# Kernel optimization log

Measured on AMD Instinct MI355X. Metric: run time of the kernel, lower is better.

The kernel has to match this reference:

```python
import jax, jax.numpy as jnp
import numpy as np

N_MOL, E_MOL = 50000, 200000
N_PRO, E_PRO = 100000, 800000


def segment_softmax(e, seg, n):
    # e: [E, H] logits, softmax over edges grouped by target node `seg`
    m = jax.ops.segment_max(e, seg, num_segments=n)
    m = jnp.where(jnp.isfinite(m), m, jnp.zeros_like(m))
    ex = jnp.exp(e - m[seg])
    s = jax.ops.segment_sum(ex, seg, num_segments=n)
    return ex / (s[seg] + 1e-16)


def gat_conv(x, edge_index, W, a_src, a_dst, b, heads, out_ch):
    # torch_geometric GATConv (concat=True, add_self_loops=True, neg slope 0.2, eval mode)
    n = x.shape[0]
    loop = jnp.arange(n, dtype=edge_index.dtype)
    src = jnp.concatenate([edge_index[0], loop])
    dst = jnp.concatenate([edge_index[1], loop])
    h = (x @ W).reshape(n, heads, out_ch)            # [N,H,C]
    alpha_s = jnp.sum(h * a_src, axis=-1)            # [N,H]
    alpha_d = jnp.sum(h * a_dst, axis=-1)            # [N,H]
    e = jax.nn.leaky_relu(alpha_s[src] + alpha_d[dst], 0.2)  # [E,H]
    alpha = segment_softmax(e, dst, n)               # [E,H]
    out = jax.ops.segment_sum(alpha[:, :, None] * h[src], dst, num_segments=n)  # [N,H,C]
    return out.reshape(n, heads * out_ch) + b


def gcn_conv(x, edge_index, edge_weight, W, b):
    # torch_geometric GCNConv with edge_weight (add_self_loops=True, sym norm)
    n = x.shape[0]
    loop = jnp.arange(n, dtype=edge_index.dtype)
    src = jnp.concatenate([edge_index[0], loop])
    dst = jnp.concatenate([edge_index[1], loop])
    w = jnp.concatenate([edge_weight, jnp.ones((n,), x.dtype)])
    deg = jax.ops.segment_sum(w, dst, num_segments=n)
    dinv = jnp.where(deg > 0, deg ** -0.5, jnp.zeros_like(deg))
    norm = dinv[src] * w * dinv[dst]                 # [E]
    h = x @ W                                        # [N,C]
    return jax.ops.segment_sum(norm[:, None] * h[src], dst, num_segments=n) + b


def setup_inputs() -> dict:
    key = jax.random.key(0)
    ks = iter(jax.random.split(key, 32))
    rn = lambda shape, s=0.1: jax.random.normal(next(ks), shape, dtype=jnp.float32) * s
    inp = {
        "mol_x": rn((N_MOL, 78), 1.0),
        "mol_edge_index": jax.random.randint(next(ks), (2, E_MOL), 0, N_MOL, dtype=jnp.int32),
        "pro_x": rn((N_PRO, 33), 1.0),
        "pro_edge_index": jax.random.randint(next(ks), (2, E_PRO), 0, N_PRO, dtype=jnp.int32),
        "pro_edge_weight": jax.random.uniform(next(ks), (E_PRO,), dtype=jnp.float32),
        # mol_conv1: GAT 78->78, heads=2
        "W1": rn((78, 156)), "a_src1": rn((2, 78)), "a_dst1": rn((2, 78)), "b1": jnp.zeros((156,), jnp.float32),
        # mol_conv2: GAT 156->156, heads=2
        "W2": rn((156, 312)), "a_src2": rn((2, 156)), "a_dst2": rn((2, 156)), "b2": jnp.zeros((312,), jnp.float32),
        # mol_conv3: GAT 312->312, heads=1
        "W3": rn((312, 312)), "a_src3": rn((1, 312)), "a_dst3": rn((1, 312)), "b3": jnp.zeros((312,), jnp.float32),
        # pro_conv1: GCN 33->33
        "Wp1": rn((33, 33)), "bp1": jnp.zeros((33,), jnp.float32),
        # pro_conv2: GAT 33->66, heads=2
        "Wp2": rn((33, 132)), "ap_src2": rn((2, 66)), "ap_dst2": rn((2, 66)), "bp2": jnp.zeros((132,), jnp.float32),
        # pro_conv3: GAT 132->132, heads=1
        "Wp3": rn((132, 132)), "ap_src3": rn((1, 132)), "ap_dst3": rn((1, 132)), "bp3": jnp.zeros((132,), jnp.float32),
    }
    return inp


def reference(mol_x, mol_edge_index, pro_x, pro_edge_index, pro_edge_weight,
              W1, a_src1, a_dst1, b1, W2, a_src2, a_dst2, b2, W3, a_src3, a_dst3, b3,
              Wp1, bp1, Wp2, ap_src2, ap_dst2, bp2, Wp3, ap_src3, ap_dst3, bp3):
    # mol branch (per CPI_GAT.forward): conv1 -> relu -> conv2 -> relu -> conv3
    x = jax.nn.relu(gat_conv(mol_x, mol_edge_index, W1, a_src1, a_dst1, b1, 2, 78))
    x = jax.nn.relu(gat_conv(x, mol_edge_index, W2, a_src2, a_dst2, b2, 2, 156))
    x = gat_conv(x, mol_edge_index, W3, a_src3, a_dst3, b3, 1, 312)
    # pro branch: gcn -> relu -> gat -> relu -> gat -> relu
    xt = jax.nn.relu(gcn_conv(pro_x, pro_edge_index, pro_edge_weight, Wp1, bp1))
    xt = jax.nn.relu(gat_conv(xt, pro_edge_index, Wp2, ap_src2, ap_dst2, bp2, 2, 66))
    xt = jax.nn.relu(gat_conv(xt, pro_edge_index, Wp3, ap_src3, ap_dst3, bp3, 1, 132))
    return (x, xt)
```

## Files before the change

kernel.cpp:

```cpp
#include <hip/hip_runtime.h>
#include <cstdint>
#include <cstddef>

#define WAVE 64
#define NPB 4

#define TBM 128
#define TBN 128
#define TBK 32
#define LDK 40

typedef short s16x8 __attribute__((ext_vector_type(8)));
typedef float f32x4 __attribute__((ext_vector_type(4)));

__device__ __forceinline__ unsigned short f2bf(float f) {
    unsigned int u = __float_as_uint(f);
    unsigned int r = (u + 0x7fffu + ((u >> 16) & 1u)) >> 16;
    return (unsigned short)r;
}
__device__ __forceinline__ float bf2f_lo(unsigned int v) { return __uint_as_float(v << 16); }
__device__ __forceinline__ float bf2f_hi(unsigned int v) { return __uint_as_float(v & 0xffff0000u); }
__device__ __forceinline__ float lrelu02(float e) { return (e > 0.f) ? e : 0.2f * e; }


__device__ __forceinline__ void gemm_body(const unsigned short* __restrict__ A,
                                          const unsigned short* __restrict__ BT,
                                          unsigned short* __restrict__ Cbf,
                                          float* __restrict__ asb, float* __restrict__ adb,
                                          const float* __restrict__ bias, int relu, int zpadTo,
                                          int N, int Kp, int M, int Mext, int Mp, int H,
                                          int bx, int by) {
    __shared__ __align__(16) unsigned short As[TBM * LDK];
    __shared__ __align__(16) unsigned short Bs[TBN * LDK];
    int tid = threadIdx.x;
    int wave = tid >> 6;
    int lane = tid & 63;
    int rowBase = by * TBM;
    int colBase = bx * TBN;
    int wm = (wave & 1) * 64;
    int wn = (wave >> 1) * 64;
    int l15 = lane & 15;
    int quad = lane >> 4;

    f32x4 acc[4][4];
    f32x4 z4 = {0.f, 0.f, 0.f, 0.f};
#pragma unroll
    for (int i = 0; i < 4; i++)
#pragma unroll
        for (int j = 0; j < 4; j++) acc[i][j] = z4;

    int srow = tid >> 2;
    int skg = tid & 3;
    const uint4 zero16 = {0u, 0u, 0u, 0u};

    for (int k0 = 0; k0 < Kp; k0 += TBK) {
#pragma unroll
        for (int half = 0; half < 2; half++) {
            int row = srow + half * 64;
            int gk = k0 + skg * 8;
            bool kok = (gk < Kp);
            {
                int gr = rowBase + row;
                uint4 v = zero16;
                if (kok && gr < N) v = *(const uint4*)(A + (size_t)gr * Kp + gk);
                *(uint4*)(As + row * LDK + skg * 8) = v;
            }
            {
                int gc = colBase + row;
                uint4 v = zero16;
                if (kok && gc < Mext) v = *(const uint4*)(BT + (size_t)gc * Kp + gk);
                *(uint4*)(Bs + row * LDK + skg * 8) = v;
            }
        }
        __syncthreads();

        s16x8 af[4], bfr[4];
#pragma unroll
        for (int mt = 0; mt < 4; mt++)
            af[mt] = *(const s16x8*)(As + (wm + mt * 16 + l15) * LDK + quad * 8);
#pragma unroll
        for (int nt = 0; nt < 4; nt++)
            bfr[nt] = *(const s16x8*)(Bs + (wn + nt * 16 + l15) * LDK + quad * 8);
#pragma unroll
        for (int mt = 0; mt < 4; mt++)
#pragma unroll
            for (int nt = 0; nt < 4; nt++)
                acc[mt][nt] = __builtin_amdgcn_mfma_f32_16x16x32_bf16(af[mt], bfr[nt], acc[mt][nt], 0, 0, 0);
        __syncthreads();
    }

#pragma unroll
    for (int mt = 0; mt < 4; mt++) {
#pragma unroll
        for (int r = 0; r < 4; r++) {
            int row = rowBase + wm + mt * 16 + quad * 4 + r;
            if (row < N) {
#pragma unroll
                for (int nt = 0; nt < 4; nt++) {
                    int col = colBase + wn + nt * 16 + l15;
                    float v = acc[mt][nt][r];
                    if (col < M) {
                        float v2 = v;
                        if (bias != nullptr) {
                            v2 += bias[col];
                            if (relu) v2 = fmaxf(v2, 0.f);
                        }
                        Cbf[(size_t)row * Mp + col] = f2bf(v2);
                    } else if (col < zpadTo) {
                        Cbf[(size_t)row * Mp + col] = 0;
                    } else if (asb != nullptr && col < M + 2 * H) {
                        int t = col - M;
                        if (t < H) asb[(size_t)row * H + t] = v;
                        else adb[(size_t)row * H + (t - H)] = v;
                    }
                }
            }
        }
    }
}


template <int SLOTS, int NG, int H, bool SM, int SWEEPS, bool GCN, bool NEXTA>
__device__ __forceinline__ void agg_gp(const unsigned short* __restrict__ hfeat,
                                       const float* __restrict__ as_, const float* __restrict__ ad_,
                                       const float* __restrict__ dinv,
                                       const int* __restrict__ rowp, const int2* __restrict__ cpack,
                                       const float* __restrict__ bias,
                                       float* __restrict__ out_f, unsigned short* __restrict__ out_bf,
                                       const float* __restrict__ vanf, int vald,
                                       float* __restrict__ asn, float* __restrict__ adn_o,
                                       int HC, int ldo, int relu, int nbase, int lane, int N) {
    constexpr int ROWB = SWEEPS * SLOTS * 16;
    int g = lane / SLOTS;
    int slot = lane - g * SLOTS;
    int n = nbase + g;
    if (g >= NG || n >= N) return;
    int C = HC / H;
    int beg = rowp[n], end = rowp[n + 1];

    float adn[H], msub[H];
    float di = 0.f, sfw;
    if (GCN) {
        di = dinv[n];
        sfw = di * di;
    } else {
#pragma unroll
        for (int h = 0; h < H; h++) {
            adn[h] = ad_[(size_t)n * H + h];
            msub[h] = lrelu02(as_[(size_t)n * H + h] + adn[h]);
        }
        sfw = 1.f;
    }

    int ch0[SWEEPS];
    bool h1q[SWEEPS][4];
#pragma unroll
    for (int sw = 0; sw < SWEEPS; sw++) {
        ch0[sw] = (sw * SLOTS + slot) * 8;
#pragma unroll
        for (int q = 0; q < 4; q++) h1q[sw][q] = (H == 2) && ((ch0[sw] + 2 * q) >= C);
    }

    float accx[SWEEPS][4], accy[SWEEPS][4];
#pragma unroll
    for (int sw = 0; sw < SWEEPS; sw++) {
        uint4 v = *(const uint4*)((const char*)hfeat + (size_t)n * ROWB + (sw * SLOTS + slot) * 16);
        unsigned int vv[4] = {v.x, v.y, v.z, v.w};
#pragma unroll
        for (int q = 0; q < 4; q++) { accx[sw][q] = sfw * bf2f_lo(vv[q]); accy[sw][q] = sfw * bf2f_hi(vv[q]); }
    }

    float wsum[H];
#pragma unroll
    for (int h = 0; h < H; h++) wsum[h] = 0.f;

    int p = beg;
    for (; p + 1 < end; p += 2) {
        int2 pk0 = cpack[p];
        int2 pk1 = cpack[p + 1];
        int s0 = pk0.x, s1 = pk1.x;
        float w0[H], w1[H];
        if (GCN) {
            w0[0] = dinv[s0] * __int_as_float(pk0.y) * di;
            w1[0] = dinv[s1] * __int_as_float(pk1.y) * di;
        } else {
#pragma unroll
            for (int h = 0; h < H; h++) {
                w0[h] = __expf(lrelu02(as_[(size_t)s0 * H + h] + adn[h]) - msub[h]);
                w1[h] = __expf(lrelu02(as_[(size_t)s1 * H + h] + adn[h]) - msub[h]);
            }
        }
        if (SM) {
#pragma unroll
            for (int h = 0; h < H; h++) wsum[h] += w0[h] + w1[h];
        }
        uint4 v0[SWEEPS], v1[SWEEPS];
#pragma unroll
        for (int sw = 0; sw < SWEEPS; sw++)
            v0[sw] = *(const uint4*)((const char*)hfeat + (size_t)s0 * ROWB + (sw * SLOTS + slot) * 16);
#pragma unroll
        for (int sw = 0; sw < SWEEPS; sw++)
            v1[sw] = *(const uint4*)((const char*)hfeat + (size_t)s1 * ROWB + (sw * SLOTS + slot) * 16);
#pragma unroll
        for (int sw = 0; sw < SWEEPS; sw++) {
            unsigned int a0[4] = {v0[sw].x, v0[sw].y, v0[sw].z, v0[sw].w};
            unsigned int a1[4] = {v1[sw].x, v1[sw].y, v1[sw].z, v1[sw].w};
#pragma unroll
            for (int q = 0; q < 4; q++) {
                float wq0 = (H == 2) ? (h1q[sw][q] ? w0[1] : w0[0]) : w0[0];
                float wq1 = (H == 2) ? (h1q[sw][q] ? w1[1] : w1[0]) : w1[0];
                accx[sw][q] += wq0 * bf2f_lo(a0[q]) + wq1 * bf2f_lo(a1[q]);
                accy[sw][q] += wq0 * bf2f_hi(a0[q]) + wq1 * bf2f_hi(a1[q]);
            }
        }
    }
    if (p < end) {
        int2 pk0 = cpack[p];
        int s0 = pk0.x;
        float w0[H];
        if (GCN) {
            w0[0] = dinv[s0] * __int_as_float(pk0.y) * di;
        } else {
#pragma unroll
            for (int h = 0; h < H; h++)
                w0[h] = __expf(lrelu02(as_[(size_t)s0 * H + h] + adn[h]) - msub[h]);
        }
        if (SM) {
#pragma unroll
            for (int h = 0; h < H; h++) wsum[h] += w0[h];
        }
        uint4 v0[SWEEPS];
#pragma unroll
        for (int sw = 0; sw < SWEEPS; sw++)
            v0[sw] = *(const uint4*)((const char*)hfeat + (size_t)s0 * ROWB + (sw * SLOTS + slot) * 16);
#pragma unroll
        for (int sw = 0; sw < SWEEPS; sw++) {
            unsigned int a0[4] = {v0[sw].x, v0[sw].y, v0[sw].z, v0[sw].w};
#pragma unroll
            for (int q = 0; q < 4; q++) {
                float wq0 = (H == 2) ? (h1q[sw][q] ? w0[1] : w0[0]) : w0[0];
                accx[sw][q] += wq0 * bf2f_lo(a0[q]);
                accy[sw][q] += wq0 * bf2f_hi(a0[q]);
            }
        }
    }

    float rs[H];
    if (SM) {
#pragma unroll
        for (int h = 0; h < H; h++) rs[h] = 1.f / (1.f + wsum[h] + 1e-16f);
    } else {
#pragma unroll
        for (int h = 0; h < H; h++) rs[h] = 1.f;
    }

    float ps[4] = {0.f, 0.f, 0.f, 0.f};
#pragma unroll
    for (int sw = 0; sw < SWEEPS; sw++) {
        float o[8];
#pragma unroll
        for (int q = 0; q < 4; q++) {
            float r = (H == 2) ? (h1q[sw][q] ? rs[1] : rs[0]) : rs[0];
            int c0 = ch0[sw] + 2 * q;
            float b0 = (c0 < HC) ? bias[c0] : 0.f;
            float b1v = (c0 + 1 < HC) ? bias[c0 + 1] : 0.f;
            float o0 = accx[sw][q] * r + b0;
            float o1 = accy[sw][q] * r + b1v;
            if (relu) { o0 = fmaxf(o0, 0.f); o1 = fmaxf(o1, 0.f); }
            if (c0 >= HC) o0 = 0.f;
            if (c0 + 1 >= HC) o1 = 0.f;
            o[2 * q] = o0;
            o[2 * q + 1] = o1;
        }
        if (NEXTA) {
#pragma unroll
            for (int j = 0; j < 8; j++) {
                int c = ch0[sw] + j;
#pragma unroll
                for (int th = 0; th < 4; th++) ps[th] += o[j] * vanf[th * vald + c];
            }
        }
        if (out_bf) {
            uint4 pk;
            unsigned* pp = (unsigned*)&pk;
#pragma unroll
            for (int q = 0; q < 4; q++)
                pp[q] = (unsigned)f2bf(o[2 * q]) | ((unsigned)f2bf(o[2 * q + 1]) << 16);
            *(uint4*)((char*)out_bf + (size_t)n * ((size_t)ldo * 2) + (sw * SLOTS + slot) * 16) = pk;
        } else {
#pragma unroll
            for (int half = 0; half < 2; half++) {
                int c0 = ch0[sw] + half * 4;
                if (c0 < HC) {
                    float4 f4 = make_float4(o[half * 4], o[half * 4 + 1], o[half * 4 + 2], o[half * 4 + 3]);
                    *(float4*)(out_f + (size_t)n * HC + c0) = f4;
                }
            }
        }
    }
    if (NEXTA) {
        constexpr int P = SLOTS >= 32 ? 32 : SLOTS >= 16 ? 16 : SLOTS >= 8 ? 8 : SLOTS >= 4 ? 4 : SLOTS >= 2 ? 2 : 1;
        if (P < SLOTS) {
#pragma unroll
            for (int th = 0; th < 4; th++) {
                float t = __shfl_down(ps[th], P);
                if (slot + P < SLOTS) ps[th] += t;
            }
        }
#pragma unroll
        for (int off = P >> 1; off > 0; off >>= 1) {
#pragma unroll
            for (int th = 0; th < 4; th++) {
                float t = __shfl_down(ps[th], off);
                if (slot + off < P) ps[th] += t;
            }
        }
        if (slot == 0) {
            asn[(size_t)n * 2 + 0] = ps[0];
            asn[(size_t)n * 2 + 1] = ps[1];
            adn_o[(size_t)n * 2 + 0] = ps[2];
            adn_o[(size_t)n * 2 + 1] = ps[3];
        }
    }
}


template <int SLOTS, int NG>
__device__ __forceinline__ void aggN_gp(const unsigned short* __restrict__ x,
                                        const float* __restrict__ as_, const float* __restrict__ ad_,
                                        const int* __restrict__ rowp, const int2* __restrict__ cpack,
                                        unsigned short* __restrict__ A2, int nbase, int lane, int N) {
    constexpr int ROWB = SLOTS * 16;
    int g = lane / SLOTS;
    int slot = lane - g * SLOTS;
    int n = nbase + g;
    if (g >= NG || n >= N) return;
    int beg = rowp[n], end = rowp[n + 1];

    float adn[2], msub[2];
#pragma unroll
    for (int h = 0; h < 2; h++) {
        adn[h] = ad_[(size_t)n * 2 + h];
        msub[h] = lrelu02(as_[(size_t)n * 2 + h] + adn[h]);
    }

    float ax[2][4], ay[2][4];
    {
        uint4 v = *(const uint4*)((const char*)x + (size_t)n * ROWB + slot * 16);
        unsigned int vv[4] = {v.x, v.y, v.z, v.w};
#pragma unroll
        for (int q = 0; q < 4; q++) {
            float lo = bf2f_lo(vv[q]), hi = bf2f_hi(vv[q]);
            ax[0][q] = lo; ax[1][q] = lo;
            ay[0][q] = hi; ay[1][q] = hi;
        }
    }
    float wsum[2] = {0.f, 0.f};

    int p = beg;
    for (; p + 1 < end; p += 2) {
        int s0 = cpack[p].x;
        int s1 = cpack[p + 1].x;
        float w0[2], w1[2];
#pragma unroll
        for (int h = 0; h < 2; h++) {
            w0[h] = __expf(lrelu02(as_[(size_t)s0 * 2 + h] + adn[h]) - msub[h]);
            w1[h] = __expf(lrelu02(as_[(size_t)s1 * 2 + h] + adn[h]) - msub[h]);
        }
        wsum[0] += w0[0] + w1[0];
        wsum[1] += w0[1] + w1[1];
        uint4 v0 = *(const uint4*)((const char*)x + (size_t)s0 * ROWB + slot * 16);
        uint4 v1 = *(const uint4*)((const char*)x + (size_t)s1 * ROWB + slot * 16);
        unsigned int a0[4] = {v0.x, v0.y, v0.z, v0.w};
        unsigned int a1[4] = {v1.x, v1.y, v1.z, v1.w};
#pragma unroll
        for (int q = 0; q < 4; q++) {
            float lo0 = bf2f_lo(a0[q]), hi0 = bf2f_hi(a0[q]);
            float lo1 = bf2f_lo(a1[q]), hi1 = bf2f_hi(a1[q]);
            ax[0][q] += w0[0] * lo0 + w1[0] * lo1;
            ax[1][q] += w0[1] * lo0 + w1[1] * lo1;
            ay[0][q] += w0[0] * hi0 + w1[0] * hi1;
            ay[1][q] += w0[1] * hi0 + w1[1] * hi1;
        }
    }
    if (p < end) {
        int s0 = cpack[p].x;
        float w0[2];
#pragma unroll
        for (int h = 0; h < 2; h++)
            w0[h] = __expf(lrelu02(as_[(size_t)s0 * 2 + h] + adn[h]) - msub[h]);
        wsum[0] += w0[0];
        wsum[1] += w0[1];
        uint4 v0 = *(const uint4*)((const char*)x + (size_t)s0 * ROWB + slot * 16);
        unsigned int a0[4] = {v0.x, v0.y, v0.z, v0.w};
#pragma unroll
        for (int q = 0; q < 4; q++) {
            float lo0 = bf2f_lo(a0[q]), hi0 = bf2f_hi(a0[q]);
            ax[0][q] += w0[0] * lo0;
            ax[1][q] += w0[1] * lo0;
            ay[0][q] += w0[0] * hi0;
            ay[1][q] += w0[1] * hi0;
        }
    }

    float rs[2];
#pragma unroll
    for (int h = 0; h < 2; h++) rs[h] = 1.f / (1.f + wsum[h] + 1e-16f);

#pragma unroll
    for (int h = 0; h < 2; h++) {
        uint4 pk;
        unsigned* pp = (unsigned*)&pk;
#pragma unroll
        for (int q = 0; q < 4; q++) {
            float o0 = ax[h][q] * rs[h];
            float o1 = ay[h][q] * rs[h];
            pp[q] = (unsigned)f2bf(o0) | ((unsigned)f2bf(o1) << 16);
        }
        *(uint4*)((char*)A2 + (size_t)n * (2 * ROWB) + h * ROWB + slot * 16) = pk;
    }
}


__device__ __forceinline__ void cvtw1(const float* __restrict__ W, unsigned short* __restrict__ WT,
                                      int K, int M, int Kp, int i) {
    int m = i / Kp;
    int k = i - m * Kp;
    WT[i] = (k < K) ? f2bf(W[(long long)k * M + m]) : (unsigned short)0;
}

__device__ __forceinline__ void cvtw_bd(const float* __restrict__ W, unsigned short* __restrict__ WT,
                                        int K, int M, int C, int Kp, int Kph, int i) {
    int m = i / Kp;
    int k = i - m * Kp;
    unsigned short v = 0;
    if (m < M) {
        int hm = m / C;
        int kk = k - hm * Kph;
        if (kk >= 0 && kk < K) v = f2bf(W[(long long)kk * M + m]);
    }
    WT[i] = v;
}

__device__ __forceinline__ void prep1(const float* __restrict__ W, const float* __restrict__ a_src,
                                      const float* __restrict__ a_dst, unsigned short* __restrict__ WT,
                                      int K, int M, int C, int Kp, int H, int b, int lane) {
    int k = b % Kp;
    int th = b / Kp;
    int t = th / H;
    int h = th - t * H;
    size_t orow = (size_t)(M + t * H + h) * Kp;
    if (k >= K) {
        if (lane == 0) WT[orow + k] = 0;
        return;
    }
    const float* a = t ? a_dst : a_src;
    int hoff = h * C;
    const float* wrow = W + (size_t)k * M + hoff;
    float acc = 0.f;
    for (int c = lane; c < C; c += 64) acc += wrow[c] * a[hoff + c];
    for (int off = 32; off > 0; off >>= 1) acc += __shfl_down(acc, off);
    if (lane == 0) WT[orow + k] = f2bf(acc);
}

__device__ __forceinline__ void prep1f(const float* __restrict__ W, const float* __restrict__ a_src,
                                       const float* __restrict__ a_dst, float* __restrict__ fout,
                                       int K, int M, int C, int Kp, int H, int b, int lane) {
    int k = b % Kp;
    int th = b / Kp;
    int t = th / H;
    int h = th - t * H;
    if (k >= K) {
        if (lane == 0) fout[(size_t)th * Kp + k] = 0.f;
        return;
    }
    const float* a = t ? a_dst : a_src;
    int hoff = h * C;
    const float* wrow = W + (size_t)k * M + hoff;
    float acc = 0.f;
    for (int c = lane; c < C; c += 64) acc += wrow[c] * a[hoff + c];
    for (int off = 32; off > 0; off >>= 1) acc += __shfl_down(acc, off);
    if (lane == 0) fout[(size_t)th * Kp + k] = acc;
}


__global__ __launch_bounds__(256) void k_A(
    const int* __restrict__ mol_dst, const int* __restrict__ pro_dst, int* __restrict__ cnt,
    int N_MOL, int E_MOL, int ET, int nb1,
    const float* __restrict__ W1, const float* __restrict__ W2, const float* __restrict__ W3,
    const float* __restrict__ Wp1, const float* __restrict__ Wp2, const float* __restrict__ Wp3,
    unsigned short* __restrict__ wt1, unsigned short* __restrict__ wt2bd, unsigned short* __restrict__ wt3,
    unsigned short* __restrict__ wtp1, unsigned short* __restrict__ wtp2bd, unsigned short* __restrict__ wtp3,
    const float* __restrict__ as1, const float* __restrict__ ad1,
    const float* __restrict__ as2, const float* __restrict__ ad2,
    const float* __restrict__ as3, const float* __restrict__ ad3,
    const float* __restrict__ aps2, const float* __restrict__ apd2,
    const float* __restrict__ aps3, const float* __restrict__ apd3,
    float* __restrict__ va2f, float* __restrict__ vap2f,
    const float* __restrict__ mol_x, unsigned short* __restrict__ xb,
    const float* __restrict__ pro_x, unsigned short* __restrict__ xpp,
    long long totM, long long totP) {
    const int nb2 = 957;
    const int nb3 = 508;
    int b = blockIdx.x;
    int tid = threadIdx.x;
    if (b < nb1) {
        int i0 = b * 1024 + tid;
#pragma unroll
        for (int k = 0; k < 4; k++) {
            int e = i0 + k * 256;
            if (e < ET) {
                int d = (e < E_MOL) ? mol_dst[e] : (N_MOL + pro_dst[e - E_MOL]);
                atomicAdd(&cnt[d], 1);
            }
        }
    } else if (b < nb1 + nb2) {
        int idx = (b - nb1) * 256 + tid;
        if (idx < 12480)        cvtw1(W1, wt1, 78, 156, 80, idx);
        else if (idx < 114880)  cvtw_bd(W2, wt2bd, 156, 312, 156, 320, 160, idx - 12480);
        else if (idx < 214720)  cvtw1(W3, wt3, 312, 312, 320, idx - 114880);
        else if (idx < 216040)  cvtw1(Wp1, wtp1, 33, 33, 40, idx - 214720);
        else if (idx < 226920)  cvtw_bd(Wp2, wtp2bd, 33, 132, 66, 80, 40, idx - 216040);
        else if (idx < 244872)  cvtw1(Wp3, wtp3, 132, 132, 136, idx - 226920);
    } else if (b < nb1 + nb2 + nb3) {
        int unit = (b - nb1 - nb2) * 4 + (tid >> 6);
        int lane = tid & 63;
        if (unit < 320)        prep1(W1, as1, ad1, wt1, 78, 156, 78, 80, 2, unit, lane);
        else if (unit < 960)   prep1f(W2, as2, ad2, va2f, 156, 312, 156, 160, 2, unit - 320, lane);
        else if (unit < 1600)  prep1(W3, as3, ad3, wt3, 312, 312, 312, 320, 1, unit - 960, lane);
        else if (unit < 1760)  prep1f(Wp2, aps2, apd2, vap2f, 33, 132, 66, 40, 2, unit - 1600, lane);
        else if (unit < 2032)  prep1(Wp3, aps3, apd3, wtp3, 132, 132, 132, 136, 1, unit - 1760, lane);
    } else {
        long long i0 = (long long)(b - nb1 - nb2 - nb3) * 1024 + tid;
#pragma unroll
        for (int k = 0; k < 4; k++) {
            long long idx = i0 + k * 256;
            if (idx < totM) {
                int n = (int)(idx / 80);
                int kk = (int)(idx - (long long)n * 80);
                xb[idx] = (kk < 78) ? f2bf(mol_x[(long long)n * 78 + kk]) : (unsigned short)0;
            } else if (idx < totM + totP) {
                long long i2 = idx - totM;
                int n = (int)(i2 / 40);
                int kk = (int)(i2 - (long long)n * 40);
                xpp[i2] = (kk < 33) ? f2bf(pro_x[(long long)n * 33 + kk]) : (unsigned short)0;
            }
        }
    }
}


__global__ __launch_bounds__(256) void k_scan1(const int* __restrict__ cnt, int* __restrict__ incl,
                                               int* __restrict__ bsums, int n) {
    __shared__ int sm[256];
    int i = blockIdx.x * 256 + threadIdx.x;
    int v = (i < n) ? cnt[i] : 0;
    sm[threadIdx.x] = v;
    __syncthreads();
    for (int off = 1; off < 256; off <<= 1) {
        int t = (threadIdx.x >= off) ? sm[threadIdx.x - off] : 0;
        __syncthreads();
        sm[threadIdx.x] += t;
        __syncthreads();
    }
    if (i < n) incl[i] = sm[threadIdx.x];
    if (threadIdx.x == 255) bsums[blockIdx.x] = sm[255];
}

__global__ __launch_bounds__(1024) void k_scan2(int* __restrict__ bsums, int nb) {
    __shared__ int sm[1024];
    int v = (threadIdx.x < nb) ? bsums[threadIdx.x] : 0;
    sm[threadIdx.x] = v;
    __syncthreads();
    for (int off = 1; off < 1024; off <<= 1) {
        int t = (threadIdx.x >= off) ? sm[threadIdx.x - off] : 0;
        __syncthreads();
        sm[threadIdx.x] += t;
        __syncthreads();
    }
    if (threadIdx.x < nb) bsums[threadIdx.x] = sm[threadIdx.x] - v;
}

__global__ __launch_bounds__(256) void k_scan3_all(const int* __restrict__ incl, const int* __restrict__ cnt,
                                                   const int* __restrict__ boff,
                                                   int* __restrict__ mol_rowp, int* __restrict__ pro_rowp,
                                                   int* __restrict__ cur,
                                                   int N_MOL, int N_PRO, int E_MOL, int E_PRO) {
    int i = blockIdx.x * 256 + threadIdx.x;
    int NT = N_MOL + N_PRO;
    if (i < NT) {
        int ex = incl[i] - cnt[i] + boff[blockIdx.x];
        cur[i] = ex;
        if (i < N_MOL) mol_rowp[i] = ex;
        else pro_rowp[i - N_MOL] = ex - E_MOL;
    }
    if (i == 0) {
        mol_rowp[N_MOL] = E_MOL;
        pro_rowp[N_PRO] = E_PRO;
    }
}


__global__ __launch_bounds__(256) void k_B(
    const int* __restrict__ msrc, const int* __restrict__ mdst,
    const int* __restrict__ psrc, const int* __restrict__ pdst,
    const float* __restrict__ pw, int* __restrict__ cur, int2* __restrict__ cpack,
    int N_MOL, int E_MOL, int ET, int nbs,
    const unsigned short* __restrict__ A1, const unsigned short* __restrict__ B1,
    unsigned short* __restrict__ C1, float* __restrict__ as1o, float* __restrict__ ad1o,
    const float* __restrict__ bias1, int relu1, int zpad1,
    int N1, int Kp1, int M1, int Mext1, int Mp1, int H1, int g1x, int nb1,
    const unsigned short* __restrict__ A2, const unsigned short* __restrict__ B2,
    unsigned short* __restrict__ C2, float* __restrict__ as2o, float* __restrict__ ad2o,
    const float* __restrict__ bias2, int relu2, int zpad2,
    int N2, int Kp2, int M2, int Mext2, int Mp2, int H2, int g2x) {
    int b = blockIdx.x;
    if (b < nbs) {
        int e = b * 256 + threadIdx.x;
        if (e < ET) {
            int s, d;
            int wbits = 0;
            if (e >= E_MOL) {
                int ep = e - E_MOL;
                s = psrc[ep];
                d = N_MOL + pdst[ep];
                wbits = __float_as_int(pw[ep]);
            } else {
                s = msrc[e];
                d = mdst[e];
            }
            int pos = atomicAdd(&cur[d], 1);
            int2 pk;
            pk.x = s;
            pk.y = wbits;
            cpack[pos] = pk;
        }
    } else if (b < nbs + nb1) {
        int bb = b - nbs;
        gemm_body(A1, B1, C1, as1o, ad1o, bias1, relu1, zpad1, N1, Kp1, M1, Mext1, Mp1, H1, bb % g1x, bb / g1x);
    } else {
        int bb = b - nbs - nb1;
        gemm_body(A2, B2, C2, as2o, ad2o, bias2, relu2, zpad2, N2, Kp2, M2, Mext2, Mp2, H2, bb % g2x, bb / g2x);
    }
}


__global__ __launch_bounds__(256) void k_deg(const int* __restrict__ rowp, const int2* __restrict__ cpack,
                                             float* __restrict__ dinv, int N) {
    int n = blockIdx.x * 256 + threadIdx.x;
    if (n < N) {
        int b = rowp[n], e = rowp[n + 1];
        float s = 0.f;
        for (int p = b; p < e; p++) s += __int_as_float(cpack[p].y);
        dinv[n] = rsqrtf(s + 1.0f);
    }
}


__global__ __launch_bounds__(NPB * 64) void k_fuse1(
    const unsigned short* __restrict__ hb, const float* __restrict__ asm_, const float* __restrict__ adm_,
    const int* __restrict__ mrowp, const int2* __restrict__ mcp, const float* __restrict__ b1,
    unsigned short* __restrict__ x2m, const float* __restrict__ va2f,
    float* __restrict__ asm2, float* __restrict__ adm2, int Nm,
    const unsigned short* __restrict__ hbp, const float* __restrict__ dinv,
    const int* __restrict__ prowp, const int2* __restrict__ pcp, const float* __restrict__ bp1,
    unsigned short* __restrict__ x2p, const float* __restrict__ vap2f,
    float* __restrict__ asp2, float* __restrict__ adp2, int Np, int nb1) {
    int wave = threadIdx.x >> 6, lane = threadIdx.x & 63;
    int b = blockIdx.x;
    if (b < nb1) {
        int nbase = (b * NPB + wave) * 3;
        agg_gp<20, 3, 2, true, 1, false, true>(hb, asm_, adm_, nullptr, mrowp, mcp, b1,
                                               nullptr, x2m, va2f, 160, asm2, adm2,
                                               156, 160, 1, nbase, lane, Nm);
    } else {
        int nbase = ((b - nb1) * NPB + wave) * 12;
        agg_gp<5, 12, 1, false, 1, true, true>(hbp, nullptr, nullptr, dinv, prowp, pcp, bp1,
                                               nullptr, x2p, vap2f, 40, asp2, adp2,
                                               33, 40, 1, nbase, lane, Np);
    }
}

__global__ __launch_bounds__(NPB * 64) void k_fuseN(
    const unsigned short* __restrict__ x2m, const float* __restrict__ asm2, const float* __restrict__ adm2,
    const int* __restrict__ mrowp, const int2* __restrict__ mcp, unsigned short* __restrict__ xa2m, int Nm,
    const unsigned short* __restrict__ x2p, const float* __restrict__ asp2, const float* __restrict__ adp2,
    const int* __restrict__ prowp, const int2* __restrict__ pcp, unsigned short* __restrict__ xa2p, int Np,
    int nb1) {
    int wave = threadIdx.x >> 6, lane = threadIdx.x & 63;
    int b = blockIdx.x;
    if (b < nb1) {
        int nbase = (b * NPB + wave) * 3;
        aggN_gp<20, 3>(x2m, asm2, adm2, mrowp, mcp, xa2m, nbase, lane, Nm);
    } else {
        int nbase = ((b - nb1) * NPB + wave) * 12;
        aggN_gp<5, 12>(x2p, asp2, adp2, prowp, pcp, xa2p, nbase, lane, Np);
    }
}

__global__ __launch_bounds__(NPB * 64) void k_fuse5(
    const unsigned short* __restrict__ hb, const float* __restrict__ asm_, const float* __restrict__ adm_,
    const int* __restrict__ mrowp, const int2* __restrict__ mcp, const float* __restrict__ b3,
    float* __restrict__ out_mol, int Nm,
    const unsigned short* __restrict__ hbp, const float* __restrict__ asp_, const float* __restrict__ adp_,
    const int* __restrict__ prowp, const int2* __restrict__ pcp, const float* __restrict__ bp3,
    float* __restrict__ out_pro, int Np, int nb1) {
    int wave = threadIdx.x >> 6, lane = threadIdx.x & 63;
    int b = blockIdx.x;
    if (b < nb1) {
        int nbase = (b * NPB + wave) * 3;
        agg_gp<20, 3, 1, true, 2, false, false>(hb, asm_, adm_, nullptr, mrowp, mcp, b3,
                                                out_mol, nullptr, nullptr, 0, nullptr, nullptr,
                                                312, 320, 0, nbase, lane, Nm);
    } else {
        int nbase = ((b - nb1) * NPB + wave) * 3;
        agg_gp<17, 3, 1, true, 1, false, false>(hbp, asp_, adp_, nullptr, prowp, pcp, bp3,
                                                out_pro, nullptr, nullptr, 0, nullptr, nullptr,
                                                132, 136, 1, nbase, lane, Np);
    }
}


extern "C" void kernel_launch(void* const* d_in, const int* in_sizes, int n_in,
                              void* d_out, int out_size, void* d_ws, size_t ws_size,
                              hipStream_t stream) {
    const int N_MOL = in_sizes[0] / 78;
    const int E_MOL = in_sizes[1] / 2;
    const int N_PRO = in_sizes[2] / 33;
    const int E_PRO = in_sizes[3] / 2;
    const int NT = N_MOL + N_PRO;
    const int ET = E_MOL + E_PRO;

    const float* mol_x = (const float*)d_in[0];
    const int* mol_ei = (const int*)d_in[1];
    const float* pro_x = (const float*)d_in[2];
    const int* pro_ei = (const int*)d_in[3];
    const float* pro_ew = (const float*)d_in[4];
    const float *W1 = (const float*)d_in[5], *as1 = (const float*)d_in[6], *ad1 = (const float*)d_in[7],
                *b1 = (const float*)d_in[8];
    const float *W2 = (const float*)d_in[9], *as2 = (const float*)d_in[10], *ad2 = (const float*)d_in[11],
                *b2 = (const float*)d_in[12];
    const float *W3 = (const float*)d_in[13], *as3 = (const float*)d_in[14], *ad3 = (const float*)d_in[15],
                *b3 = (const float*)d_in[16];
    const float *Wp1 = (const float*)d_in[17], *bp1 = (const float*)d_in[18];
    const float *Wp2 = (const float*)d_in[19], *aps2 = (const float*)d_in[20], *apd2 = (const float*)d_in[21],
                *bp2 = (const float*)d_in[22];
    const float *Wp3 = (const float*)d_in[23], *aps3 = (const float*)d_in[24], *apd3 = (const float*)d_in[25],
                *bp3 = (const float*)d_in[26];

    float* out_mol = (float*)d_out;
    float* out_pro = (float*)d_out + (size_t)N_MOL * 312;

    char* ob = (char*)d_out;
    size_t o_xa2m = 0;
    size_t o_xa2p = o_xa2m + (size_t)N_MOL * 320 * 2;
    size_t o_xb0  = o_xa2p + (size_t)N_PRO * 80 * 2;
    size_t o_xp0  = o_xb0 + (size_t)N_MOL * 80 * 2;
    size_t o_xpp  = o_xp0 + (size_t)N_PRO * 40 * 2;
    unsigned short* xa2m = (unsigned short*)(ob + o_xa2m);
    unsigned short* xa2p = (unsigned short*)(ob + o_xa2p);
    unsigned short* xb0  = (unsigned short*)(ob + o_xb0);
    unsigned short* xp0  = (unsigned short*)(ob + o_xp0);
    unsigned short* xpp  = (unsigned short*)(ob + o_xpp);

    char* p = (char*)d_ws;
    auto alloc = [&](size_t bytes) -> void* {
        void* r = (void*)p;
        p += (bytes + 255) & ~(size_t)255;
        return r;
    };
    int* cnt_all  = (int*)alloc((size_t)NT * 4);
    int* incl     = (int*)alloc((size_t)NT * 4);
    int* cur_all  = (int*)alloc((size_t)NT * 4);
    int* bsums    = (int*)alloc(1024 * 4);
    int* mol_rowp = (int*)alloc((size_t)(N_MOL + 1) * 4);
    int* pro_rowp = (int*)alloc((size_t)(N_PRO + 1) * 4);
    int2* cpack   = (int2*)alloc((size_t)ET * 8);
    float* dinv   = (float*)alloc((size_t)N_PRO * 4);
    float* asb_m  = (float*)alloc((size_t)N_MOL * 2 * 4);
    float* adb_m  = (float*)alloc((size_t)N_MOL * 2 * 4);
    float* asb_m2 = (float*)alloc((size_t)N_MOL * 2 * 4);
    float* adb_m2 = (float*)alloc((size_t)N_MOL * 2 * 4);
    float* asb_p  = (float*)alloc((size_t)N_PRO * 2 * 4);
    float* adb_p  = (float*)alloc((size_t)N_PRO * 2 * 4);
    float* asb_p2 = (float*)alloc((size_t)N_PRO * 2 * 4);
    float* adb_p2 = (float*)alloc((size_t)N_PRO * 2 * 4);
    float* va2f   = (float*)alloc((size_t)4 * 160 * 4);
    float* vap2f  = (float*)alloc((size_t)4 * 40 * 4);
    unsigned short* bufA = (unsigned short*)alloc((size_t)N_MOL * 320 * 2);
    unsigned short* bufB = (unsigned short*)alloc((size_t)N_MOL * 320 * 2);
    unsigned short* bufC = (unsigned short*)alloc((size_t)N_PRO * 136 * 2);
    unsigned short* wt1    = (unsigned short*)alloc((size_t)160 * 80 * 2);
    unsigned short* wt2bd  = (unsigned short*)alloc((size_t)320 * 320 * 2);
    unsigned short* wt3    = (unsigned short*)alloc((size_t)320 * 320 * 2);
    unsigned short* wtp1   = (unsigned short*)alloc((size_t)40 * 40 * 2);
    unsigned short* wtp2bd = (unsigned short*)alloc((size_t)136 * 80 * 2);
    unsigned short* wtp3   = (unsigned short*)alloc((size_t)136 * 136 * 2);
    (void)ws_size;

    unsigned short* hb1  = bufA;
    unsigned short* x3m  = bufA;
    unsigned short* x2m  = bufB;
    unsigned short* x2p  = bufB + (size_t)N_MOL * 160;
    unsigned short* hb3  = bufB;
    unsigned short* hbp1 = bufC;
    unsigned short* hbp3 = bufC;

    int2* mol_cp = cpack;
    int2* pro_cp = cpack + E_MOL;

    const int* mol_src = mol_ei;
    const int* mol_dst = mol_ei + E_MOL;
    const int* pro_src = pro_ei;
    const int* pro_dst = pro_ei + E_PRO;

    const long long totM = (long long)N_MOL * 80;
    const long long totP = (long long)N_PRO * 40;

    hipMemsetAsync(cnt_all, 0, (size_t)NT * 4, stream);
    int nbCnt = (ET + 1023) / 1024;
    int nbCvx = (int)((totM + totP + 1023) / 1024);
    int gridA = nbCnt + 957 + 508 + nbCvx;
    k_A<<<gridA, 256, 0, stream>>>(mol_dst, pro_dst, cnt_all, N_MOL, E_MOL, ET, nbCnt,
                                   W1, W2, W3, Wp1, Wp2, Wp3, wt1, wt2bd, wt3, wtp1, wtp2bd, wtp3,
                                   as1, ad1, as2, ad2, as3, ad3, aps2, apd2, aps3, apd3,
                                   va2f, vap2f, mol_x, xb0, pro_x, xp0, totM, totP);

    int nbT = (NT + 255) / 256;
    k_scan1<<<nbT, 256, 0, stream>>>(cnt_all, incl, bsums, NT);
    k_scan2<<<1, 1024, 0, stream>>>(bsums, nbT);
    k_scan3_all<<<nbT, 256, 0, stream>>>(incl, cnt_all, bsums, mol_rowp, pro_rowp, cur_all,
                                         N_MOL, N_PRO, E_MOL, E_PRO);

    int gyM = (N_MOL + TBM - 1) / TBM;
    int gyP = (N_PRO + TBM - 1) / TBM;

    {
        int nbs = (ET + 255) / 256;
        int g1x = 2;
        int nb1 = g1x * gyM;
        int g2x = 1;
        k_B<<<nbs + nb1 + g2x * gyP, 256, 0, stream>>>(
            mol_src, mol_dst, pro_src, pro_dst, pro_ew, cur_all, cpack, N_MOL, E_MOL, ET, nbs,
            xb0, wt1, hb1, asb_m, adb_m, nullptr, 0, 0, N_MOL, 80, 156, 160, 160, 2, g1x, nb1,
            xp0, wtp1, hbp1, nullptr, nullptr, nullptr, 0, 0, N_PRO, 40, 33, 33, 40, 0, g2x);
    }

    k_deg<<<(N_PRO + 255) / 256, 256, 0, stream>>>(pro_rowp, pro_cp, dinv, N_PRO);

    {
        int nb1 = (N_MOL + NPB * 3 - 1) / (NPB * 3);
        int nb2 = (N_PRO + NPB * 12 - 1) / (NPB * 12);
        k_fuse1<<<nb1 + nb2, NPB * 64, 0, stream>>>(hb1, asb_m, adb_m, mol_rowp, mol_cp, b1,
                                                    x2m, va2f, asb_m2, adb_m2, N_MOL,
                                                    hbp1, dinv, pro_rowp, pro_cp, bp1,
                                                    x2p, vap2f, asb_p2, adb_p2, N_PRO, nb1);
    }

    {
        int nb1 = (N_MOL + NPB * 3 - 1) / (NPB * 3);
        int nb2 = (N_PRO + NPB * 12 - 1) / (NPB * 12);
        k_fuseN<<<nb1 + nb2, NPB * 64, 0, stream>>>(x2m, asb_m2, adb_m2, mol_rowp, mol_cp, xa2m, N_MOL,
                                                    x2p, asb_p2, adb_p2, pro_rowp, pro_cp, xa2p, N_PRO, nb1);
    }

    {
        int g1x = 3;
        int nb1 = g1x * gyM;
        int g2x = 2;
        k_B<<<nb1 + g2x * gyP, 256, 0, stream>>>(
            nullptr, nullptr, nullptr, nullptr, nullptr, nullptr, nullptr, N_MOL, E_MOL, ET, 0,
            xa2m, wt2bd, x3m, nullptr, nullptr, b2, 1, 320, N_MOL, 320, 312, 320, 320, 0, g1x, nb1,
            xa2p, wtp2bd, xpp, nullptr, nullptr, bp2, 1, 136, N_PRO, 80, 132, 136, 136, 0, g2x);
    }

    {
        int g1x = 3;
        int nb1 = g1x * gyM;
        int g2x = 2;
        k_B<<<nb1 + g2x * gyP, 256, 0, stream>>>(
            nullptr, nullptr, nullptr, nullptr, nullptr, nullptr, nullptr, N_MOL, E_MOL, ET, 0,
            x3m, wt3, hb3, asb_m, adb_m, nullptr, 0, 0, N_MOL, 320, 312, 314, 320, 1, g1x, nb1,
            xpp, wtp3, hbp3, asb_p, adb_p, nullptr, 0, 0, N_PRO, 136, 132, 134, 136, 1, g2x);
    }

    {
        int nb1 = (N_MOL + NPB * 3 - 1) / (NPB * 3);
        int nb2 = (N_PRO + NPB * 3 - 1) / (NPB * 3);
        k_fuse5<<<nb1 + nb2, NPB * 64, 0, stream>>>(hb3, asb_m, adb_m, mol_rowp, mol_cp, b3, out_mol, N_MOL,
                                                    hbp3, asb_p, adb_p, pro_rowp, pro_cp, bp3, out_pro, N_PRO, nb1);
    }
}
```

Before: 707.1 us.

## Replace direct CSR edge scatter with two-pass bucketed scatter

After: 694.9 us, median of 2. Within noise of the previous version (-1.7%).

```diff
diff --git a/kernel.cpp b/kernel.cpp
--- a/kernel.cpp
+++ b/kernel.cpp
@@ -487,6 +487,7 @@
 __global__ __launch_bounds__(256) void k_A(
     const int* __restrict__ mol_dst, const int* __restrict__ pro_dst, int* __restrict__ cnt,
     int N_MOL, int E_MOL, int ET, int nb1,
+    int* __restrict__ hist, int NBLK, int NBUK, int SH, int ROUNDS,
     const float* __restrict__ W1, const float* __restrict__ W2, const float* __restrict__ W3,
     const float* __restrict__ Wp1, const float* __restrict__ Wp2, const float* __restrict__ Wp3,
     unsigned short* __restrict__ wt1, unsigned short* __restrict__ wt2bd, unsigned short* __restrict__ wt3,
@@ -504,6 +505,7 @@
     const int nb3 = 508;
     int b = blockIdx.x;
     int tid = threadIdx.x;
+    __shared__ int lhist[256];
     if (b < nb1) {
         int i0 = b * 1024 + tid;
 #pragma unroll
@@ -514,16 +516,30 @@
                 atomicAdd(&cnt[d], 1);
             }
         }
-    } else if (b < nb1 + nb2) {
-        int idx = (b - nb1) * 256 + tid;
+    } else if (b < nb1 + NBLK) {
+        int eb = b - nb1;
+        lhist[tid] = 0;
+        __syncthreads();
+        int base = eb * (ROUNDS * 256);
+        for (int r = 0; r < ROUNDS; r++) {
+            int e = base + r * 256 + tid;
+            if (e < ET) {
+                int d = (e < E_MOL) ? mol_dst[e] : (N_MOL + pro_dst[e - E_MOL]);
+                atomicAdd(&lhist[d >> SH], 1);
+            }
+        }
+        __syncthreads();
+        if (tid < NBUK) hist[tid * NBLK + eb] = lhist[tid];
+    } else if (b < nb1 + NBLK + nb2) {
+        int idx = (b - nb1 - NBLK) * 256 + tid;
         if (idx < 12480)        cvtw1(W1, wt1, 78, 156, 80, idx);
         else if (idx < 114880)  cvtw_bd(W2, wt2bd, 156, 312, 156, 320, 160, idx - 12480);
         else if (idx < 214720)  cvtw1(W3, wt3, 312, 312, 320, idx - 114880);
         else if (idx < 216040)  cvtw1(Wp1, wtp1, 33, 33, 40, idx - 214720);
         else if (idx < 226920)  cvtw_bd(Wp2, wtp2bd, 33, 132, 66, 80, 40, idx - 216040);
         else if (idx < 244872)  cvtw1(Wp3, wtp3, 132, 132, 136, idx - 226920);
-    } else if (b < nb1 + nb2 + nb3) {
-        int unit = (b - nb1 - nb2) * 4 + (tid >> 6);
+    } else if (b < nb1 + NBLK + nb2 + nb3) {
+        int unit = (b - nb1 - NBLK - nb2) * 4 + (tid >> 6);
         int lane = tid & 63;
         if (unit < 320)        prep1(W1, as1, ad1, wt1, 78, 156, 78, 80, 2, unit, lane);
         else if (unit < 960)   prep1f(W2, as2, ad2, va2f, 156, 312, 156, 160, 2, unit - 320, lane);
@@ -531,7 +547,7 @@
         else if (unit < 1760)  prep1f(Wp2, aps2, apd2, vap2f, 33, 132, 66, 40, 2, unit - 1600, lane);
         else if (unit < 2032)  prep1(Wp3, aps3, apd3, wtp3, 132, 132, 132, 136, 1, unit - 1760, lane);
     } else {
-        long long i0 = (long long)(b - nb1 - nb2 - nb3) * 1024 + tid;
+        long long i0 = (long long)(b - nb1 - NBLK - nb2 - nb3) * 1024 + tid;
 #pragma unroll
         for (int k = 0; k < 4; k++) {
             long long idx = i0 + k * 256;
@@ -601,11 +617,31 @@
 }
 
 
+__global__ __launch_bounds__(256) void k_histscan(int* __restrict__ hist, const int* __restrict__ cur,
+                                                  int NBLK, int SH, int NT, int ET) {
+    __shared__ int sm[256];
+    int b = blockIdx.x;
+    int t = threadIdx.x;
+    int v = (t < NBLK) ? hist[b * NBLK + t] : 0;
+    sm[t] = v;
+    __syncthreads();
+    for (int off = 1; off < 256; off <<= 1) {
+        int x = (t >= off) ? sm[t - off] : 0;
+        __syncthreads();
+        sm[t] += x;
+        __syncthreads();
+    }
+    int node = b << SH;
+    int base = (node < NT) ? cur[node] : ET;
+    if (t < NBLK) hist[b * NBLK + t] = base + sm[t] - v;
+}
+
+
 __global__ __launch_bounds__(256) void k_B(
     const int* __restrict__ msrc, const int* __restrict__ mdst,
     const int* __restrict__ psrc, const int* __restrict__ pdst,
-    const float* __restrict__ pw, int* __restrict__ cur, int2* __restrict__ cpack,
-    int N_MOL, int E_MOL, int ET, int nbs,
+    const float* __restrict__ pw, const int* __restrict__ blockstart, int2* __restrict__ ebkt,
+    int N_MOL, int E_MOL, int ET, int nbs, int NBLK, int NBUK, int SH, int ROUNDS,
     const unsigned short* __restrict__ A1, const unsigned short* __restrict__ B1,
     unsigned short* __restrict__ C1, float* __restrict__ as1o, float* __restrict__ ad1o,
     const float* __restrict__ bias1, int relu1, int zpad1,
@@ -616,24 +652,33 @@
     int N2, int Kp2, int M2, int Mext2, int Mp2, int H2, int g2x) {
     int b = blockIdx.x;
     if (b < nbs) {
-        int e = b * 256 + threadIdx.x;
-        if (e < ET) {
-            int s, d;
-            int wbits = 0;
-            if (e >= E_MOL) {
-                int ep = e - E_MOL;
-                s = psrc[ep];
-                d = N_MOL + pdst[ep];
-                wbits = __float_as_int(pw[ep]);
-            } else {
-                s = msrc[e];
-                d = mdst[e];
-            }
-            int pos = atomicAdd(&cur[d], 1);
-            int2 pk;
-            pk.x = s;
-            pk.y = wbits;
-            cpack[pos] = pk;
+        __shared__ int lofs[256];
+        int eb = b;
+        int tid = threadIdx.x;
+        if (tid < NBUK) lofs[tid] = blockstart[tid * NBLK + eb];
+        __syncthreads();
+        int base = eb * (ROUNDS * 256);
+        for (int r = 0; r < ROUNDS; r++) {
+            int e = base + r * 256 + tid;
+            if (e < ET) {
+                int s, d;
+                int wbits = 0;
+                if (e >= E_MOL) {
+                    int ep = e - E_MOL;
+                    s = psrc[ep];
+                    d = N_MOL + pdst[ep];
+                    wbits = __float_as_int(pw[ep]);
+                } else {
+                    s = msrc[e];
+                    d = mdst[e];
+                }
+                int bk = d >> SH;
+                int pos = atomicAdd(&lofs[bk], 1);
+                int2 pk;
+                pk.x = s | ((d - (bk << SH)) << 18);
+                pk.y = wbits;
+                ebkt[pos] = pk;
+            }
         }
     } else if (b < nbs + nb1) {
         int bb = b - nbs;
@@ -641,6 +686,26 @@
     } else {
         int bb = b - nbs - nb1;
         gemm_body(A2, B2, C2, as2o, ad2o, bias2, relu2, zpad2, N2, Kp2, M2, Mext2, Mp2, H2, bb % g2x, bb / g2x);
+    }
+}
+
+
+__global__ __launch_bounds__(256) void k_pass2(const int2* __restrict__ ebkt, const int* __restrict__ blockstart,
+                                               int* __restrict__ cur, int2* __restrict__ cpack,
+                                               int NBUK, int NBLK, int SH, int ET) {
+    int b = blockIdx.x >> 3;
+    int s = blockIdx.x & 7;
+    int start = blockstart[b * NBLK];
+    int end = (b + 1 < NBUK) ? blockstart[(b + 1) * NBLK] : ET;
+    for (int i = start + s * 256 + threadIdx.x; i < end; i += 8 * 256) {
+        int2 pk = ebkt[i];
+        int src = pk.x & 0x3FFFF;
+        int d = (b << SH) | ((unsigned)pk.x >> 18);
+        int pos = atomicAdd(&cur[d], 1);
+        int2 o;
+        o.x = src;
+        o.y = pk.y;
+        cpack[pos] = o;
     }
 }
 
@@ -751,6 +816,14 @@
     float* out_mol = (float*)d_out;
     float* out_pro = (float*)d_out + (size_t)N_MOL * 312;
 
+    int SH = 10;
+    while (((NT + (1 << SH) - 1) >> SH) > 256) SH++;
+    const int NBUK = (NT + (1 << SH) - 1) >> SH;
+    int ROUNDS = (ET + 65535) / 65536;
+    if (ROUNDS < 16) ROUNDS = 16;
+    const int EB = ROUNDS * 256;
+    const int NBLK = (ET + EB - 1) / EB;
+
     char* ob = (char*)d_out;
     size_t o_xa2m = 0;
     size_t o_xa2p = o_xa2m + (size_t)N_MOL * 320 * 2;
@@ -776,6 +849,8 @@
     int* mol_rowp = (int*)alloc((size_t)(N_MOL + 1) * 4);
     int* pro_rowp = (int*)alloc((size_t)(N_PRO + 1) * 4);
     int2* cpack   = (int2*)alloc((size_t)ET * 8);
+    int2* ebkt    = (int2*)alloc((size_t)ET * 8);
+    int* hist     = (int*)alloc((size_t)256 * 256 * 4);
     float* dinv   = (float*)alloc((size_t)N_PRO * 4);
     float* asb_m  = (float*)alloc((size_t)N_MOL * 2 * 4);
     float* adb_m  = (float*)alloc((size_t)N_MOL * 2 * 4);
@@ -820,8 +895,9 @@
     hipMemsetAsync(cnt_all, 0, (size_t)NT * 4, stream);
     int nbCnt = (ET + 1023) / 1024;
     int nbCvx = (int)((totM + totP + 1023) / 1024);
-    int gridA = nbCnt + 957 + 508 + nbCvx;
+    int gridA = nbCnt + NBLK + 957 + 508 + nbCvx;
     k_A<<<gridA, 256, 0, stream>>>(mol_dst, pro_dst, cnt_all, N_MOL, E_MOL, ET, nbCnt,
+                                   hist, NBLK, NBUK, SH, ROUNDS,
                                    W1, W2, W3, Wp1, Wp2, Wp3, wt1, wt2bd, wt3, wtp1, wtp2bd, wtp3,
                                    as1, ad1, as2, ad2, as3, ad3, aps2, apd2, aps3, apd3,
                                    va2f, vap2f, mol_x, xb0, pro_x, xp0, totM, totP);
@@ -832,19 +908,23 @@
     k_scan3_all<<<nbT, 256, 0, stream>>>(incl, cnt_all, bsums, mol_rowp, pro_rowp, cur_all,
                                          N_MOL, N_PRO, E_MOL, E_PRO);
 
+    k_histscan<<<NBUK, 256, 0, stream>>>(hist, cur_all, NBLK, SH, NT, ET);
+
     int gyM = (N_MOL + TBM - 1) / TBM;
     int gyP = (N_PRO + TBM - 1) / TBM;
 
     {
-        int nbs = (ET + 255) / 256;
         int g1x = 2;
         int nb1 = g1x * gyM;
         int g2x = 1;
-        k_B<<<nbs + nb1 + g2x * gyP, 256, 0, stream>>>(
-            mol_src, mol_dst, pro_src, pro_dst, pro_ew, cur_all, cpack, N_MOL, E_MOL, ET, nbs,
+        k_B<<<NBLK + nb1 + g2x * gyP, 256, 0, stream>>>(
+            mol_src, mol_dst, pro_src, pro_dst, pro_ew, hist, ebkt,
+            N_MOL, E_MOL, ET, NBLK, NBLK, NBUK, SH, ROUNDS,
             xb0, wt1, hb1, asb_m, adb_m, nullptr, 0, 0, N_MOL, 80, 156, 160, 160, 2, g1x, nb1,
             xp0, wtp1, hbp1, nullptr, nullptr, nullptr, 0, 0, N_PRO, 40, 33, 33, 40, 0, g2x);
     }
+
+    k_pass2<<<NBUK * 8, 256, 0, stream>>>(ebkt, hist, cur_all, cpack, NBUK, NBLK, SH, ET);
 
     k_deg<<<(N_PRO + 255) / 256, 256, 0, stream>>>(pro_rowp, pro_cp, dinv, N_PRO);
 
@@ -869,7 +949,8 @@
         int nb1 = g1x * gyM;
         int g2x = 2;
         k_B<<<nb1 + g2x * gyP, 256, 0, stream>>>(
-            nullptr, nullptr, nullptr, nullptr, nullptr, nullptr, nullptr, N_MOL, E_MOL, ET, 0,
+            nullptr, nullptr, nullptr, nullptr, nullptr, nullptr, nullptr,
+            N_MOL, E_MOL, ET, 0, NBLK, NBUK, SH, ROUNDS,
             xa2m, wt2bd, x3m, nullptr, nullptr, b2, 1, 320, N_MOL, 320, 312, 320, 320, 0, g1x, nb1,
             xa2p, wtp2bd, xpp, nullptr, nullptr, bp2, 1, 136, N_PRO, 80, 132, 136, 136, 0, g2x);
     }
@@ -879,7 +960,8 @@
         int nb1 = g1x * gyM;
         int g2x = 2;
         k_B<<<nb1 + g2x * gyP, 256, 0, stream>>>(
-            nullptr, nullptr, nullptr, nullptr, nullptr, nullptr, nullptr, N_MOL, E_MOL, ET, 0,
+            nullptr, nullptr, nullptr, nullptr, nullptr, nullptr, nullptr,
+            N_MOL, E_MOL, ET, 0, NBLK, NBUK, SH, ROUNDS,
             x3m, wt3, hb3, asb_m, adb_m, nullptr, 0, 0, N_MOL, 320, 312, 314, 320, 1, g1x, nb1,
             xpp, wtp3, hbp3, asb_p, adb_p, nullptr, 0, 0, N_PRO, 136, 132, 134, 136, 1, g2x);
     }
```
